# Performance work log

Measured on AMD Instinct MI355X. Metric: run time of the kernel, lower is better.

## Reference

```python
import jax, jax.numpy as jnp
import numpy as np

K = 3      # kernel size
PAD = 1    # kernel_size // 2


def _deform_conv(x, offset, w_def):
    """mmcv DeformConv (deform_groups=1, stride=1, dilation=1, no bias).
    x: [B,C,H,W], offset: [B,2*K*K,H,W] ordered (dy,dx) per kernel tap, w_def: [O,C,K,K].
    Bilinear sampling with zero padding outside the feature map.
    """
    B, C, H, W = x.shape
    kk = K * K
    off = offset.reshape(B, kk, 2, H, W)
    # kernel-tap grid (row-major: ky, kx)
    ar = jnp.arange(K)
    gy, gx = jnp.meshgrid(ar, ar, indexing='ij')
    gy = gy.reshape(kk)
    gx = gx.reshape(kk)
    hh = jnp.arange(H, dtype=x.dtype)
    ww = jnp.arange(W, dtype=x.dtype)
    # sampling positions: p0 - pad + kernel tap + learned offset  -> [B,kk,H,W]
    ys = hh[None, None, :, None] - PAD + gy[None, :, None, None] + off[:, :, 0]
    xs = ww[None, None, None, :] - PAD + gx[None, :, None, None] + off[:, :, 1]

    y0 = jnp.floor(ys)
    x0 = jnp.floor(xs)
    ly = ys - y0
    lx = xs - x0

    xf = x.reshape(B, C, H * W)

    def gather(yi, xi):
        valid = (yi >= 0) & (yi <= H - 1) & (xi >= 0) & (xi <= W - 1)
        yc = jnp.clip(yi, 0, H - 1).astype(jnp.int32)
        xc = jnp.clip(xi, 0, W - 1).astype(jnp.int32)
        idx = (yc * W + xc).reshape(B, 1, kk * H * W)
        g = jnp.take_along_axis(xf, idx, axis=2).reshape(B, C, kk, H, W)
        return g * valid.reshape(B, 1, kk, H, W).astype(x.dtype)

    # bilinear interpolation, per-corner zero masking == zero padding
    v = (gather(y0, x0) * ((1 - ly) * (1 - lx))[:, None]
         + gather(y0, x0 + 1) * ((1 - ly) * lx)[:, None]
         + gather(y0 + 1, x0) * (ly * (1 - lx))[:, None]
         + gather(y0 + 1, x0 + 1) * (ly * lx)[:, None])  # [B,C,kk,H,W]

    O = w_def.shape[0]
    return jnp.einsum('bckhw,ock->bohw', v, w_def.reshape(O, C, kk))


def setup_inputs() -> dict:
    key = jax.random.key(0)
    k1, k2, k3, k4 = jax.random.split(key, 4)
    B, C_in, C_off, C_out, H, W = 4, 128, 64, 128, 128, 128
    x = jax.random.normal(k1, (B, C_in, H, W), dtype=jnp.float32)
    off = jax.random.normal(k2, (B, C_off, H, W), dtype=jnp.float32)
    # NOTE: the torch module zero-inits the offset conv; we use small random
    # weights so the deformable gather path is actually exercised.
    w_off = 0.1 * jax.random.normal(k3, (2 * K * K, C_off), dtype=jnp.float32)
    b_off = jnp.zeros((2 * K * K,), dtype=jnp.float32)
    w_def = jax.random.normal(k4, (C_out, C_in, K, K), dtype=jnp.float32) / np.sqrt(C_in * K * K)
    return {"x": x, "off": off, "w_off": w_off, "b_off": b_off, "w_def": w_def}


def reference(x, off, w_off, b_off, w_def):
    # 1x1 offset conv
    offset = jnp.einsum('oc,bchw->bohw', w_off, off) + b_off[None, :, None, None]
    # deformable conv + ReLU
    return jax.nn.relu(_deform_conv(x, offset, w_def))
```

## Files before the change

kernel.cpp:

```cpp
#include <hip/hip_runtime.h>
#include <stdint.h>

typedef __attribute__((ext_vector_type(8))) short short8;
typedef __attribute__((ext_vector_type(4))) float f32x4;

constexpr int Hc = 128, Wc = 128, HWc = Hc * Wc;
constexpr int Cin = 128, Cout = 128;
constexpr int OffC = 18, OffIn = 64;

__device__ __forceinline__ float bf2f(unsigned short u) {
    return __builtin_bit_cast(float, (unsigned)u << 16);
}
__device__ __forceinline__ unsigned short f2bf(float f) {
    unsigned u = __builtin_bit_cast(unsigned, f);
    return (unsigned short)((u + 0x7FFFu + ((u >> 16) & 1u)) >> 16);
}

__global__ void k_offconv(const float* __restrict__ off, const float* __restrict__ w_off,
                          const float* __restrict__ b_off, float* __restrict__ offset) {
    __shared__ float wsm[OffC * OffIn];
    __shared__ float bsm[OffC];
    int tid = threadIdx.x;
    for (int i = tid; i < OffC * OffIn; i += 256) wsm[i] = w_off[i];
    if (tid < OffC) bsm[tid] = b_off[tid];
    __syncthreads();
    int g = (blockIdx.x * 256 + tid) * 4;
    int b = g >> 14, hw = g & (HWc - 1);
    const float* offb = off + b * OffIn * HWc + hw;
    float acc[OffC][4];
#pragma unroll
    for (int o = 0; o < OffC; ++o) {
        float bv = bsm[o];
        acc[o][0] = bv; acc[o][1] = bv; acc[o][2] = bv; acc[o][3] = bv;
    }
    for (int c = 0; c < OffIn; ++c) {
        float4 v = *(const float4*)(offb + (c << 14));
#pragma unroll
        for (int o = 0; o < OffC; ++o) {
            float wv = wsm[o * OffIn + c];
            acc[o][0] += wv * v.x; acc[o][1] += wv * v.y;
            acc[o][2] += wv * v.z; acc[o][3] += wv * v.w;
        }
    }
    float* outb = offset + b * OffC * HWc + hw;
#pragma unroll
    for (int o = 0; o < OffC; ++o) {
        float4 v; v.x = acc[o][0]; v.y = acc[o][1]; v.z = acc[o][2]; v.w = acc[o][3];
        *(float4*)(outb + (o << 14)) = v;
    }
}

__global__ void k_xpose(const float* __restrict__ x, unsigned short* __restrict__ xt) {
    __shared__ float tile[128][65];
    int blk = blockIdx.x;
    int b = blk >> 8;
    int hw0 = (blk & 255) << 6;
    const float* xb = x + b * Cin * HWc;
    int tid = threadIdx.x;
#pragma unroll
    for (int k = 0; k < 32; ++k) {
        int e = tid + k * 256;
        int c = e >> 6, p = e & 63;
        tile[c][p] = xb[(c << 14) + hw0 + p];
    }
    __syncthreads();
    unsigned short* xtb = xt + ((b << 14) + hw0) * Cin;
#pragma unroll
    for (int k = 0; k < 32; ++k) {
        int e = tid + k * 256;
        int p = e >> 7, c = e & 127;
        xtb[e] = f2bf(tile[c][p]);
    }
}

__global__ void k_wprep(const float* __restrict__ wd, unsigned short* __restrict__ wt) {
    int i = blockIdx.x * 256 + threadIdx.x;
    int kk = i >> 14, o = (i >> 7) & 127, c = i & 127;
    wt[i] = f2bf(wd[((o << 7) + c) * 9 + kk]);
}

__global__ __launch_bounds__(256)
void k_deform(const unsigned short* __restrict__ xt, const float* __restrict__ offset,
              const unsigned short* __restrict__ wt, float* __restrict__ out) {
    __shared__ float offs[OffC][64];
    __shared__ float wgt[9][4][64];
    __shared__ int cbase[9][4][64];
    __shared__ __align__(16) unsigned short vt[64 * 128];

    int tid = threadIdx.x;
    int blk = blockIdx.x;
    int b = blk >> 8;
    int hw0 = (blk & 255) << 6;

    const float* offg = offset + b * OffC * HWc + hw0;
    for (int i = tid; i < OffC * 64; i += 256)
        offs[i >> 6][i & 63] = offg[((i >> 6) << 14) + (i & 63)];
    __syncthreads();

    for (int t = tid; t < 576; t += 256) {
        int tap = t >> 6, p = t & 63;
        int hw = hw0 + p, h = hw >> 7, w = hw & 127;
        float dy = offs[2 * tap][p], dx = offs[2 * tap + 1][p];
        float ys = (float)(h - 1 + tap / 3) + dy;
        float xs = (float)(w - 1 + tap % 3) + dx;
        float y0f = floorf(ys), x0f = floorf(xs);
        float ly = ys - y0f, lx = xs - x0f;
        int y0 = (int)y0f, x0 = (int)x0f;
#pragma unroll
        for (int cr = 0; cr < 4; ++cr) {
            int yi = y0 + (cr >> 1), xi = x0 + (cr & 1);
            bool valid = (yi >= 0) && (yi < Hc) && (xi >= 0) && (xi < Wc);
            float wy = (cr >> 1) ? ly : 1.0f - ly;
            float wx = (cr & 1) ? lx : 1.0f - lx;
            int yc = yi < 0 ? 0 : (yi > Hc - 1 ? Hc - 1 : yi);
            int xc = xi < 0 ? 0 : (xi > Wc - 1 ? Wc - 1 : xi);
            wgt[tap][cr][p] = valid ? wy * wx : 0.0f;
            cbase[tap][cr][p] = ((yc << 7) + xc) << 7;
        }
    }

    f32x4 acc[2][4];
#pragma unroll
    for (int i = 0; i < 2; ++i)
#pragma unroll
        for (int j = 0; j < 4; ++j)
            acc[i][j] = (f32x4){0.f, 0.f, 0.f, 0.f};

    int lane = tid & 63, wave = tid >> 6;
    const unsigned short* xb = xt + (b << 14) * Cin;
    char* vtb = (char*)vt;
    int c4 = (tid & 31) << 2;

    for (int tap = 0; tap < 9; ++tap) {
        __syncthreads();
        for (int pass = 0; pass < 8; ++pass) {
            int p = (tid >> 5) + (pass << 3);
            float v0 = 0.f, v1 = 0.f, v2 = 0.f, v3 = 0.f;
#pragma unroll
            for (int cr = 0; cr < 4; ++cr) {
                float wc = wgt[tap][cr][p];
                const unsigned short* src = xb + cbase[tap][cr][p] + c4;
                ushort4 raw = *(const ushort4*)src;
                v0 += wc * bf2f(raw.x);
                v1 += wc * bf2f(raw.y);
                v2 += wc * bf2f(raw.z);
                v3 += wc * bf2f(raw.w);
            }
            ushort4 pk;
            pk.x = f2bf(v0); pk.y = f2bf(v1); pk.z = f2bf(v2); pk.w = f2bf(v3);
            int byteoff = ((p << 8) + (c4 << 1)) ^ ((p & 7) << 4);
            *(ushort4*)(vtb + byteoff) = pk;
        }
        __syncthreads();
        const unsigned short* wtap = wt + (tap << 14);
        int orow = wave << 5;
#pragma unroll
        for (int kb = 0; kb < 4; ++kb) {
            int kc = (kb << 5) + ((lane >> 4) << 3);
            short8 a0 = *(const short8*)(wtap + (orow + (lane & 15)) * 128 + kc);
            short8 a1 = *(const short8*)(wtap + (orow + 16 + (lane & 15)) * 128 + kc);
#pragma unroll
            for (int pb = 0; pb < 4; ++pb) {
                int p = (pb << 4) + (lane & 15);
                int byteoff = ((p << 8) + (kc << 1)) ^ ((p & 7) << 4);
                short8 bfrag = *(const short8*)(vtb + byteoff);
                acc[0][pb] = __builtin_amdgcn_mfma_f32_16x16x32_bf16(a0, bfrag, acc[0][pb], 0, 0, 0);
                acc[1][pb] = __builtin_amdgcn_mfma_f32_16x16x32_bf16(a1, bfrag, acc[1][pb], 0, 0, 0);
            }
        }
    }

    float* outb = out + (b * Cout) * HWc + hw0;
    int orow2 = wave << 5;
#pragma unroll
    for (int ob = 0; ob < 2; ++ob)
#pragma unroll
        for (int pb = 0; pb < 4; ++pb)
#pragma unroll
            for (int j = 0; j < 4; ++j) {
                int o = orow2 + (ob << 4) + ((lane >> 4) << 2) + j;
                int p = (pb << 4) + (lane & 15);
                float v = acc[ob][pb][j];
                outb[o * HWc + p] = v > 0.f ? v : 0.f;
            }
}

extern "C" void kernel_launch(void* const* d_in, const int* in_sizes, int n_in,
                              void* d_out, int out_size, void* d_ws, size_t ws_size,
                              hipStream_t stream) {
    const float* x     = (const float*)d_in[0];
    const float* off   = (const float*)d_in[1];
    const float* w_off = (const float*)d_in[2];
    const float* b_off = (const float*)d_in[3];
    const float* w_def = (const float*)d_in[4];
    float* out = (float*)d_out;

    char* ws = (char*)d_ws;
    float* offset      = (float*)ws;
    unsigned short* xt = (unsigned short*)(ws + 4718592);
    unsigned short* wt = (unsigned short*)(ws + 4718592 + 16777216);

    hipLaunchKernelGGL(k_offconv, dim3(64),   dim3(256), 0, stream, off, w_off, b_off, offset);
    hipLaunchKernelGGL(k_xpose,   dim3(1024), dim3(256), 0, stream, x, xt);
    hipLaunchKernelGGL(k_wprep,   dim3(576),  dim3(256), 0, stream, w_def, wt);
    hipLaunchKernelGGL(k_deform,  dim3(1024), dim3(256), 0, stream, xt, offset, wt, out);
}
```

Before: 214.8 us.

## Double-buffer deform gather with MFMA, enlarge tiles, widen offconv grid

The main deform kernel now processes 128 pixels per 512-thread block and double-buffers the sampled-column tile in LDS. Bilinear gathers for the next tap are issued and consumed between the MFMA halves of the current tap, so global gather latency overlaps tensor-core work. It also computes sampling parameters in registers instead of staging them through shared memory, and swizzles the block order. The offset conv uses one pixel per thread across 4x more blocks for parallelism, and the transpose writes packed bf16 pairs. The cost is higher register and LDS pressure per block, which may limit occupancy.

Measured after the change: 206.7 us. 3.8% less time.

```diff
diff --git a/kernel.cpp b/kernel.cpp
--- a/kernel.cpp
+++ b/kernel.cpp
@@ -24,30 +24,20 @@
     for (int i = tid; i < OffC * OffIn; i += 256) wsm[i] = w_off[i];
     if (tid < OffC) bsm[tid] = b_off[tid];
     __syncthreads();
-    int g = (blockIdx.x * 256 + tid) * 4;
+    int g = blockIdx.x * 256 + tid;
     int b = g >> 14, hw = g & (HWc - 1);
     const float* offb = off + b * OffIn * HWc + hw;
-    float acc[OffC][4];
-#pragma unroll
-    for (int o = 0; o < OffC; ++o) {
-        float bv = bsm[o];
-        acc[o][0] = bv; acc[o][1] = bv; acc[o][2] = bv; acc[o][3] = bv;
-    }
+    float acc[OffC];
+#pragma unroll
+    for (int o = 0; o < OffC; ++o) acc[o] = bsm[o];
     for (int c = 0; c < OffIn; ++c) {
-        float4 v = *(const float4*)(offb + (c << 14));
-#pragma unroll
-        for (int o = 0; o < OffC; ++o) {
-            float wv = wsm[o * OffIn + c];
-            acc[o][0] += wv * v.x; acc[o][1] += wv * v.y;
-            acc[o][2] += wv * v.z; acc[o][3] += wv * v.w;
-        }
+        float v = offb[c << 14];
+#pragma unroll
+        for (int o = 0; o < OffC; ++o) acc[o] += wsm[o * OffIn + c] * v;
     }
     float* outb = offset + b * OffC * HWc + hw;
 #pragma unroll
-    for (int o = 0; o < OffC; ++o) {
-        float4 v; v.x = acc[o][0]; v.y = acc[o][1]; v.z = acc[o][2]; v.w = acc[o][3];
-        *(float4*)(outb + (o << 14)) = v;
-    }
+    for (int o = 0; o < OffC; ++o) outb[o << 14] = acc[o];
 }
 
 __global__ void k_xpose(const float* __restrict__ x, unsigned short* __restrict__ xt) {
@@ -66,10 +56,12 @@
     __syncthreads();
     unsigned short* xtb = xt + ((b << 14) + hw0) * Cin;
 #pragma unroll
-    for (int k = 0; k < 32; ++k) {
-        int e = tid + k * 256;
+    for (int k = 0; k < 16; ++k) {
+        int e = (tid + k * 256) * 2;
         int p = e >> 7, c = e & 127;
-        xtb[e] = f2bf(tile[c][p]);
+        unsigned lo = f2bf(tile[c][p]);
+        unsigned hi = f2bf(tile[c + 1][p]);
+        *(unsigned*)(xtb + e) = lo | (hi << 16);
     }
 }
 
@@ -79,28 +71,33 @@
     wt[i] = f2bf(wd[((o << 7) + c) * 9 + kk]);
 }
 
-__global__ __launch_bounds__(256)
+__global__ __launch_bounds__(512, 4)
 void k_deform(const unsigned short* __restrict__ xt, const float* __restrict__ offset,
               const unsigned short* __restrict__ wt, float* __restrict__ out) {
-    __shared__ float offs[OffC][64];
-    __shared__ float wgt[9][4][64];
-    __shared__ int cbase[9][4][64];
-    __shared__ __align__(16) unsigned short vt[64 * 128];
+    __shared__ float offs[OffC][128];
+    __shared__ __align__(16) unsigned short vt[2][128 * 128];
 
     int tid = threadIdx.x;
-    int blk = blockIdx.x;
-    int b = blk >> 8;
-    int hw0 = (blk & 255) << 6;
+    int bid = blockIdx.x;
+    int swz = (bid & 7) * 64 + (bid >> 3);
+    int b = swz >> 7;
+    int hw0 = (swz & 127) << 7;
 
     const float* offg = offset + b * OffC * HWc + hw0;
-    for (int i = tid; i < OffC * 64; i += 256)
-        offs[i >> 6][i & 63] = offg[((i >> 6) << 14) + (i & 63)];
-    __syncthreads();
-
-    for (int t = tid; t < 576; t += 256) {
-        int tap = t >> 6, p = t & 63;
-        int hw = hw0 + p, h = hw >> 7, w = hw & 127;
-        float dy = offs[2 * tap][p], dx = offs[2 * tap + 1][p];
+    for (int i = tid; i < OffC * 128; i += 512)
+        offs[i >> 7][i & 127] = offg[((i >> 7) << 14) + (i & 127)];
+    __syncthreads();
+
+    int px = tid >> 2;
+    int cq = tid & 3;
+    int c0 = cq * 8;
+    int h = (hw0 + px) >> 7, w = (hw0 + px) & 127;
+    const unsigned short* xb = xt + (size_t)(b << 14) * Cin;
+    char* vtb = (char*)vt;
+
+    float cw[4]; int cb[4];
+    auto calc_params = [&](int tap) {
+        float dy = offs[2 * tap][px], dx = offs[2 * tap + 1][px];
         float ys = (float)(h - 1 + tap / 3) + dy;
         float xs = (float)(w - 1 + tap % 3) + dx;
         float y0f = floorf(ys), x0f = floorf(xs);
@@ -114,74 +111,101 @@
             float wx = (cr & 1) ? lx : 1.0f - lx;
             int yc = yi < 0 ? 0 : (yi > Hc - 1 ? Hc - 1 : yi);
             int xc = xi < 0 ? 0 : (xi > Wc - 1 ? Wc - 1 : xi);
-            wgt[tap][cr][p] = valid ? wy * wx : 0.0f;
-            cbase[tap][cr][p] = ((yc << 7) + xc) << 7;
-        }
-    }
-
-    f32x4 acc[2][4];
-#pragma unroll
-    for (int i = 0; i < 2; ++i)
-#pragma unroll
-        for (int j = 0; j < 4; ++j)
+            cw[cr] = valid ? wy * wx : 0.0f;
+            cb[cr] = ((yc << 7) + xc) << 7;
+        }
+    };
+    auto issue = [&](short8* r, int i) {
+#pragma unroll
+        for (int cr = 0; cr < 4; ++cr)
+            r[cr] = *(const short8*)(xb + cb[cr] + c0 + i * 32);
+    };
+    auto consume = [&](short8* r, int i, int buf) {
+        float v[8];
+#pragma unroll
+        for (int k = 0; k < 8; ++k) {
+            v[k] = cw[0] * bf2f((unsigned short)r[0][k])
+                 + cw[1] * bf2f((unsigned short)r[1][k])
+                 + cw[2] * bf2f((unsigned short)r[2][k])
+                 + cw[3] * bf2f((unsigned short)r[3][k]);
+        }
+        short8 pk;
+#pragma unroll
+        for (int k = 0; k < 8; ++k) pk[k] = (short)f2bf(v[k]);
+        int byteoff = ((px << 8) + ((c0 + i * 32) << 1)) ^ ((px & 7) << 4);
+        *(short8*)(vtb + buf * 32768 + byteoff) = pk;
+    };
+
+    int lane = tid & 63, wave = tid >> 6;
+    int obase = (wave >> 2) << 6;
+    int pbase = (wave & 3) << 5;
+
+    f32x4 acc[4][2];
+#pragma unroll
+    for (int i = 0; i < 4; ++i)
+#pragma unroll
+        for (int j = 0; j < 2; ++j)
             acc[i][j] = (f32x4){0.f, 0.f, 0.f, 0.f};
 
-    int lane = tid & 63, wave = tid >> 6;
-    const unsigned short* xb = xt + (b << 14) * Cin;
-    char* vtb = (char*)vt;
-    int c4 = (tid & 31) << 2;
-
-    for (int tap = 0; tap < 9; ++tap) {
+    auto mfma_half = [&](int buf, int tap, int kb0) {
+        const unsigned short* wtap = wt + (tap << 14);
+#pragma unroll
+        for (int kb = kb0; kb < kb0 + 2; ++kb) {
+            int kc = (kb << 5) + ((lane >> 4) << 3);
+            int p0 = pbase + (lane & 15);
+            int p1 = p0 + 16;
+            short8 b0 = *(const short8*)(vtb + buf * 32768 + ((((p0 << 8) + (kc << 1)) ^ ((p0 & 7) << 4))));
+            short8 b1 = *(const short8*)(vtb + buf * 32768 + ((((p1 << 8) + (kc << 1)) ^ ((p1 & 7) << 4))));
+            short8 aa[4];
+#pragma unroll
+            for (int ot = 0; ot < 4; ++ot)
+                aa[ot] = *(const short8*)(wtap + (obase + (ot << 4) + (lane & 15)) * 128 + kc);
+#pragma unroll
+            for (int ot = 0; ot < 4; ++ot) {
+                acc[ot][0] = __builtin_amdgcn_mfma_f32_16x16x32_bf16(aa[ot], b0, acc[ot][0], 0, 0, 0);
+                acc[ot][1] = __builtin_amdgcn_mfma_f32_16x16x32_bf16(aa[ot], b1, acc[ot][1], 0, 0, 0);
+            }
+        }
+    };
+
+    short8 r0[4], r1[4];
+
+    calc_params(0);
+    issue(r0, 0); issue(r1, 1);
+    consume(r0, 0, 0); issue(r0, 2);
+    consume(r1, 1, 0); issue(r1, 3);
+    consume(r0, 2, 0); consume(r1, 3, 0);
+    __syncthreads();
+
+    for (int t = 0; t < 9; ++t) {
+        int cur = t & 1;
+        if (t < 8) {
+            calc_params(t + 1);
+            issue(r0, 0); issue(r1, 1);
+        }
+        mfma_half(cur, t, 0);
+        if (t < 8) {
+            consume(r0, 0, cur ^ 1); issue(r0, 2);
+            consume(r1, 1, cur ^ 1); issue(r1, 3);
+        }
+        mfma_half(cur, t, 2);
+        if (t < 8) {
+            consume(r0, 2, cur ^ 1); consume(r1, 3, cur ^ 1);
+        }
         __syncthreads();
-        for (int pass = 0; pass < 8; ++pass) {
-            int p = (tid >> 5) + (pass << 3);
-            float v0 = 0.f, v1 = 0.f, v2 = 0.f, v3 = 0.f;
-#pragma unroll
-            for (int cr = 0; cr < 4; ++cr) {
-                float wc = wgt[tap][cr][p];
-                const unsigned short* src = xb + cbase[tap][cr][p] + c4;
-                ushort4 raw = *(const ushort4*)src;
-                v0 += wc * bf2f(raw.x);
-                v1 += wc * bf2f(raw.y);
-                v2 += wc * bf2f(raw.z);
-                v3 += wc * bf2f(raw.w);
-            }
-            ushort4 pk;
-            pk.x = f2bf(v0); pk.y = f2bf(v1); pk.z = f2bf(v2); pk.w = f2bf(v3);
-            int byteoff = ((p << 8) + (c4 << 1)) ^ ((p & 7) << 4);
-            *(ushort4*)(vtb + byteoff) = pk;
-        }
-        __syncthreads();
-        const unsigned short* wtap = wt + (tap << 14);
-        int orow = wave << 5;
-#pragma unroll
-        for (int kb = 0; kb < 4; ++kb) {
-            int kc = (kb << 5) + ((lane >> 4) << 3);
-            short8 a0 = *(const short8*)(wtap + (orow + (lane & 15)) * 128 + kc);
-            short8 a1 = *(const short8*)(wtap + (orow + 16 + (lane & 15)) * 128 + kc);
-#pragma unroll
-            for (int pb = 0; pb < 4; ++pb) {
-                int p = (pb << 4) + (lane & 15);
-                int byteoff = ((p << 8) + (kc << 1)) ^ ((p & 7) << 4);
-                short8 bfrag = *(const short8*)(vtb + byteoff);
-                acc[0][pb] = __builtin_amdgcn_mfma_f32_16x16x32_bf16(a0, bfrag, acc[0][pb], 0, 0, 0);
-                acc[1][pb] = __builtin_amdgcn_mfma_f32_16x16x32_bf16(a1, bfrag, acc[1][pb], 0, 0, 0);
-            }
-        }
-    }
-
-    float* outb = out + (b * Cout) * HWc + hw0;
-    int orow2 = wave << 5;
-#pragma unroll
-    for (int ob = 0; ob < 2; ++ob)
-#pragma unroll
-        for (int pb = 0; pb < 4; ++pb)
+    }
+
+    float* outb = out + (size_t)(b * Cout) * HWc + hw0;
+#pragma unroll
+    for (int ot = 0; ot < 4; ++ot)
+#pragma unroll
+        for (int pb = 0; pb < 2; ++pb)
 #pragma unroll
             for (int j = 0; j < 4; ++j) {
-                int o = orow2 + (ob << 4) + ((lane >> 4) << 2) + j;
-                int p = (pb << 4) + (lane & 15);
-                float v = acc[ob][pb][j];
-                outb[o * HWc + p] = v > 0.f ? v : 0.f;
+                int o = obase + (ot << 4) + ((lane >> 4) << 2) + j;
+                int p = pbase + (pb << 4) + (lane & 15);
+                float v = acc[ot][pb][j];
+                outb[(o << 14) + p] = v > 0.f ? v : 0.f;
             }
 }
 
@@ -200,8 +224,8 @@
     unsigned short* xt = (unsigned short*)(ws + 4718592);
     unsigned short* wt = (unsigned short*)(ws + 4718592 + 16777216);
 
-    hipLaunchKernelGGL(k_offconv, dim3(64),   dim3(256), 0, stream, off, w_off, b_off, offset);
+    hipLaunchKernelGGL(k_offconv, dim3(256),  dim3(256), 0, stream, off, w_off, b_off, offset);
     hipLaunchKernelGGL(k_xpose,   dim3(1024), dim3(256), 0, stream, x, xt);
     hipLaunchKernelGGL(k_wprep,   dim3(576),  dim3(256), 0, stream, w_def, wt);
-    hipLaunchKernelGGL(k_deform,  dim3(1024), dim3(256), 0, stream, xt, offset, wt, out);
-}
+    hipLaunchKernelGGL(k_deform,  dim3(512),  dim3(512), 0, stream, xt, offset, wt, out);
+}
```
